# Performance work log

Hardware: AMD Instinct MI355X
Metric: run time of the kernel (lower is better)

## Reference

```python
import jax, jax.numpy as jnp
import numpy as np

INPUT_SIZE = 128
HIDDEN_SIZE = 128
B, S = 4, 4096


def setup_inputs() -> dict:
    key = jax.random.key(0)
    ks = jax.random.split(key, 9)
    sc_in = 1.0 / np.sqrt(INPUT_SIZE)
    sc_h = 1.0 / np.sqrt(HIDDEN_SIZE)
    return {
        "x": jax.random.normal(ks[0], (B, S, INPUT_SIZE), jnp.float32),
        "Wq": jax.random.uniform(ks[1], (INPUT_SIZE, HIDDEN_SIZE), jnp.float32, -sc_in, sc_in),
        "bq": jax.random.uniform(ks[2], (HIDDEN_SIZE,), jnp.float32, -sc_in, sc_in),
        "Wk": jax.random.uniform(ks[3], (INPUT_SIZE, HIDDEN_SIZE), jnp.float32, -sc_in, sc_in),
        "bk": jax.random.uniform(ks[4], (HIDDEN_SIZE,), jnp.float32, -sc_in, sc_in),
        "Wv": jax.random.uniform(ks[5], (INPUT_SIZE, HIDDEN_SIZE), jnp.float32, -sc_in, sc_in),
        "bv": jax.random.uniform(ks[6], (HIDDEN_SIZE,), jnp.float32, -sc_in, sc_in),
        "Wo": jax.random.uniform(ks[7], (HIDDEN_SIZE, INPUT_SIZE), jnp.float32, -sc_h, sc_h),
        "bo": jax.random.uniform(ks[8], (INPUT_SIZE,), jnp.float32, -sc_h, sc_h),
    }


def reference(x, Wq, bq, Wk, bk, Wv, bv, Wo, bo):
    # single-head scaled dot-product attention (non-causal), dropout is eval-mode identity
    q = x @ Wq + bq                      # [B, S, H]
    k = x @ Wk + bk                      # [B, S, H]
    v = x @ Wv + bv                      # [B, S, H]
    scale = 1.0 / jnp.sqrt(jnp.asarray(HIDDEN_SIZE, x.dtype))
    scores = jnp.einsum("bsh,bth->bst", q, k) * scale   # [B, S, S]
    attn = jax.nn.softmax(scores, axis=-1)
    attended = jnp.einsum("bst,bth->bsh", attn, v)       # [B, S, H]
    return attended @ Wo + bo                            # [B, S, input_size]
```

## Files before the change

kernel.cpp:

```cpp
#include <hip/hip_runtime.h>
#include <stdint.h>

typedef __attribute__((ext_vector_type(8))) short short8;
typedef __attribute__((ext_vector_type(4))) float f32x4;
typedef __attribute__((ext_vector_type(16))) float f32x16;
typedef __attribute__((ext_vector_type(4))) int i32x4;
typedef __attribute__((ext_vector_type(2))) int i32x2;

#define MFMA16(a, b, c) __builtin_amdgcn_mfma_f32_16x16x32_bf16((a), (b), (c), 0, 0, 0)
#define MFMA32(a, b, c) __builtin_amdgcn_mfma_f32_32x32x16_bf16((a), (b), (c), 0, 0, 0)

typedef __attribute__((address_space(1))) const void GVoid;
typedef __attribute__((address_space(3))) void LVoid;
#define GLDS16(g, l) __builtin_amdgcn_global_load_lds((GVoid*)(g), (LVoid*)(l), 16, 0, 0)

#define L2E 1.4426950408889634f

__device__ __forceinline__ unsigned short f2bf(float f) {
  unsigned int u = __builtin_bit_cast(unsigned int, f);
  u += 0x7fffu + ((u >> 16) & 1u);
  return (unsigned short)(u >> 16);
}
__device__ __forceinline__ float bf2f(unsigned short u) {
  return __builtin_bit_cast(float, (unsigned int)u << 16);
}

__device__ __forceinline__ float fexp2(float x) {
  return __builtin_amdgcn_exp2f(x);
}

__device__ __forceinline__ i32x2 pls(int a, int b) {
  return __builtin_amdgcn_permlane32_swap(a, b, false, false);
}
__device__ __forceinline__ float fasf(int x) { return __builtin_bit_cast(float, x); }
__device__ __forceinline__ int iasi(float x) { return __builtin_bit_cast(int, x); }

__device__ __forceinline__ int cvtpk(float lo, float hi) {
  int d;
  asm("v_cvt_pk_bf16_f32 %0, %1, %2" : "=v"(d) : "v"(lo), "v"(hi));
  return d;
}

__global__ __launch_bounds__(256) void k_proj(
    const float* __restrict__ x,
    const float* __restrict__ Wq, const float* __restrict__ bq,
    const float* __restrict__ Wk, const float* __restrict__ bk,
    const float* __restrict__ Wv, const float* __restrict__ bv,
    const float* __restrict__ Wo,
    unsigned short* __restrict__ Q2, unsigned short* __restrict__ K2,
    unsigned short* __restrict__ V2, unsigned short* __restrict__ Wo2)
{
  __shared__ __align__(16) unsigned short wt[128 * 128];
  __shared__ __align__(16) unsigned short st[64 * 136];
  const int tid  = threadIdx.x;
  const int lane = tid & 63;
  const int wid  = tid >> 6;
  const int l15  = lane & 15;
  const int g    = lane >> 4;
  const int wI   = blockIdx.x >> 8;
  const int blk  = blockIdx.x & 255;
  const int r0   = blk * 64 + wid * 16;

  if (blockIdx.x == 0) {
    for (int e = tid; e < 16384; e += 256) {
      int j = e & 7, ln = (e >> 3) & 63, kt = (e >> 9) & 7, dt = e >> 12;
      int h = kt * 16 + (ln >> 5) * 8 + j, oc = dt * 32 + (ln & 31);
      Wo2[e] = f2bf(Wo[h * 128 + oc]);
    }
  }

  short8 af[4];
  {
    const float* xp = x + (r0 + l15) * 128 + g * 8;
#pragma unroll
    for (int kt = 0; kt < 4; ++kt) {
      float4 v0 = *(const float4*)(xp + kt * 32);
      float4 v1 = *(const float4*)(xp + kt * 32 + 4);
      short8 a;
      a[0] = (short)f2bf(v0.x); a[1] = (short)f2bf(v0.y);
      a[2] = (short)f2bf(v0.z); a[3] = (short)f2bf(v0.w);
      a[4] = (short)f2bf(v1.x); a[5] = (short)f2bf(v1.y);
      a[6] = (short)f2bf(v1.z); a[7] = (short)f2bf(v1.w);
      af[kt] = a;
    }
  }

  const float* W  = (wI == 0) ? Wq : (wI == 1) ? Wk : Wv;
  const float* bv_ = (wI == 0) ? bq : (wI == 1) ? bk : bv;

  for (int i = 0; i < 64; ++i) {
    int idx = i * 256 + tid;
    int k = idx >> 7, n = idx & 127;
    int cs = (k >> 3) ^ (n & 7);
    wt[n * 128 + cs * 8 + (k & 7)] = f2bf(W[idx]);
  }
  __syncthreads();

  float bias[8];
#pragma unroll
  for (int nt = 0; nt < 8; ++nt) bias[nt] = bv_[nt * 16 + l15];

  f32x4 acc[8];
#pragma unroll
  for (int nt = 0; nt < 8; ++nt) acc[nt] = (f32x4){0.f, 0.f, 0.f, 0.f};

#pragma unroll
  for (int nt = 0; nt < 8; ++nt) {
    const int n = nt * 16 + l15;
#pragma unroll
    for (int ks = 0; ks < 4; ++ks) {
      int cs = (ks * 4 + g) ^ (n & 7);
      short8 bf = *(const short8*)&wt[n * 128 + cs * 8];
      acc[nt] = MFMA16(af[ks], bf, acc[nt]);
    }
  }

  if (wI < 2) {
    const float sc = (wI == 0) ? 0.08838834764831845f : 1.0f;
#pragma unroll
    for (int nt = 0; nt < 8; ++nt) {
      int col = nt * 16 + l15;
#pragma unroll
      for (int r = 0; r < 4; ++r)
        st[(wid * 16 + g * 4 + r) * 136 + col] = f2bf((acc[nt][r] + bias[nt]) * sc);
    }
    __syncthreads();
    unsigned short* Og = (wI == 0) ? Q2 : K2;
#pragma unroll
    for (int c4 = 0; c4 < 4; ++c4) {
      int c = c4 * 256 + tid;
      int T = c >> 9, cc = c & 511;
      int kt = cc >> 6, hib = (cc >> 5) & 1, s32 = cc & 31;
      int m0 = blk * 64 + T * 32;
      int bb = m0 >> 12, tile = (m0 & 4095) >> 5;
      short8 v = *(const short8*)&st[(T * 32 + s32) * 136 + kt * 16 + hib * 8];
      *(short8*)&Og[(size_t)(bb * 128 + tile) * 4096 + cc * 8] = v;
    }
  } else {
#pragma unroll
    for (int nt = 0; nt < 8; ++nt) {
      int col = nt * 16 + l15;
      int m0 = r0 + g * 4;
      int bb = m0 >> 12, srow = m0 & 4095;
      int idx = (bb * 128 + (srow >> 5)) * 4096 + ((srow >> 4) & 1) * 2048 +
                (col >> 5) * 512 + ((srow >> 3) & 1) * 256 + (col & 31) * 8 +
                (srow & 7);
      ushort4 pk;
      pk.x = f2bf(acc[nt][0] + bias[nt]);
      pk.y = f2bf(acc[nt][1] + bias[nt]);
      pk.z = f2bf(acc[nt][2] + bias[nt]);
      pk.w = f2bf(acc[nt][3] + bias[nt]);
      *(ushort4*)&V2[idx] = pk;
    }
  }
}

__global__ __launch_bounds__(256, 2) void k_attn(
    const unsigned short* __restrict__ Q2,
    const unsigned short* __restrict__ K2,
    const unsigned short* __restrict__ V2,
    unsigned short* __restrict__ PA,
    float2* __restrict__ ML2)
{
  __shared__ __align__(16) char smem[66560];
  const int tid = threadIdx.x, lane = tid & 63, wid = tid >> 6;
  const int rr = lane & 31, hi = lane >> 5;
  const int p = blockIdx.x;
  const int b = (p & 7) >> 1;
  const int idx = ((p >> 3) << 1) | (p & 1);
  const int qst = idx >> 2, kvq = idx & 3;
  const int q0tile = qst * 4 + wid;

  short8 qf[8];
  {
    const unsigned short* qp = Q2 + (size_t)(b * 128 + q0tile) * 4096 + lane * 8;
#pragma unroll
    for (int kt = 0; kt < 8; ++kt) qf[kt] = *(const short8*)(qp + kt * 512);
  }

  const unsigned short* gsrc[4];
  gsrc[0] = K2 + (size_t)(b * 128 + kvq * 32 + 0) * 4096 + tid * 8;
  gsrc[1] = K2 + (size_t)(b * 128 + kvq * 32 + 1) * 4096 + tid * 8;
  gsrc[2] = V2 + (size_t)(b * 128 + kvq * 32 + 0) * 4096 + tid * 8;
  gsrc[3] = V2 + (size_t)(b * 128 + kvq * 32 + 1) * 4096 + tid * 8;

  char* const rbuf = smem + 65536 + wid * 128;

#pragma unroll
  for (int i = 0; i < 4; ++i) {
    GLDS16(gsrc[i], smem + i * 8192 + tid * 16);
    GLDS16(gsrc[i] + 2048, smem + i * 8192 + 4096 + tid * 16);
  }

  f32x16 O[4];
#pragma unroll
  for (int dt = 0; dt < 4; ++dt)
#pragma unroll
    for (int j = 0; j < 16; ++j) O[dt][j] = 0.f;
  f32x16 zc;
#pragma unroll
  for (int j = 0; j < 16; ++j) zc[j] = 0.f;
  float mS = -3.0e38f, lS = 0.f;

  for (int t = 0; t < 16; ++t) {
    char* const b0 = smem + (t & 1) * 32768;
    if (t < 15) {
      char* const bn = smem + ((t + 1) & 1) * 32768;
      const size_t adv = (size_t)(t + 1) * 8192;
#pragma unroll
      for (int i = 0; i < 4; ++i) {
        GLDS16(gsrc[i] + adv, bn + i * 8192 + tid * 16);
        GLDS16(gsrc[i] + adv + 2048, bn + i * 8192 + 4096 + tid * 16);
      }
      asm volatile("s_waitcnt vmcnt(8)" ::: "memory");
    } else {
      asm volatile("s_waitcnt vmcnt(0)" ::: "memory");
    }
    __builtin_amdgcn_s_barrier();
    __builtin_amdgcn_sched_barrier(0);

    f32x16 sT0, sT1;
    __builtin_amdgcn_s_setprio(1);
    {
      short8 kf[8];
#pragma unroll
      for (int kt = 0; kt < 8; ++kt)
        kf[kt] = *(const short8*)(b0 + kt * 1024 + lane * 16);
      sT0 = MFMA32(kf[0], qf[0], zc);
#pragma unroll
      for (int kt = 1; kt < 8; ++kt) sT0 = MFMA32(kf[kt], qf[kt], sT0);
    }
    {
      short8 kf[8];
#pragma unroll
      for (int kt = 0; kt < 8; ++kt)
        kf[kt] = *(const short8*)(b0 + 8192 + kt * 1024 + lane * 16);
      sT1 = MFMA32(kf[0], qf[0], zc);
#pragma unroll
      for (int kt = 1; kt < 8; ++kt) sT1 = MFMA32(kf[kt], qf[kt], sT1);
    }
    __builtin_amdgcn_s_setprio(0);

    {
      float pm = fmaxf(fmaxf(fmaxf(sT0[0], sT0[1]), fmaxf(sT0[2], sT0[3])),
                       fmaxf(fmaxf(sT0[4], sT0[5]), fmaxf(sT0[6], sT0[7])));
      pm = fmaxf(pm, fmaxf(fmaxf(fmaxf(sT0[8], sT0[9]), fmaxf(sT0[10], sT0[11])),
                           fmaxf(fmaxf(sT0[12], sT0[13]), fmaxf(sT0[14], sT0[15]))));
      { i32x2 r = pls(iasi(pm), iasi(pm)); pm = fmaxf(fasf(r[0]), fasf(r[1])); }

      if (!__all(pm - mS <= 8.0f)) {
        float mnew = fmaxf(mS, pm);
        float fsc = fexp2((mS - mnew) * L2E);
        mS = mnew;
        lS *= fsc;
        if (hi == 0) *(float*)(rbuf + rr * 4) = fsc;
        f32x4 fr[4];
#pragma unroll
        for (int i = 0; i < 4; ++i)
          fr[i] = *(const f32x4*)(rbuf + i * 32 + hi * 16);
#pragma unroll
        for (int dt = 0; dt < 4; ++dt)
#pragma unroll
          for (int i = 0; i < 4; ++i)
#pragma unroll
            for (int j = 0; j < 4; ++j) O[dt][i * 4 + j] *= fr[i][j];
      }

      const float mL = mS * L2E;
      float pv[16];
#pragma unroll
      for (int r = 0; r < 16; ++r) pv[r] = fexp2(sT0[r] * L2E - mL);
      float s01 = (pv[0] + pv[1]) + (pv[2] + pv[3]);
      float s23 = (pv[4] + pv[5]) + (pv[6] + pv[7]);
      float s45 = (pv[8] + pv[9]) + (pv[10] + pv[11]);
      float s67 = (pv[12] + pv[13]) + (pv[14] + pv[15]);
      float ts = (s01 + s23) + (s45 + s67);
      { i32x2 r = pls(iasi(ts), iasi(ts)); ts = fasf(r[0]) + fasf(r[1]); }
      lS += ts;

      short8 pa0, pa1;
      {
        int dw[8];
#pragma unroll
        for (int m = 0; m < 8; ++m) dw[m] = cvtpk(pv[2 * m], pv[2 * m + 1]);
        i32x2 ra = pls(dw[0], dw[2]);
        i32x2 rb = pls(dw[1], dw[3]);
        i32x2 rc = pls(dw[4], dw[6]);
        i32x2 rd = pls(dw[5], dw[7]);
        i32x4 w0 = {ra[0], rb[0], ra[1], rb[1]};
        i32x4 w1 = {rc[0], rd[0], rc[1], rd[1]};
        pa0 = __builtin_bit_cast(short8, w0);
        pa1 = __builtin_bit_cast(short8, w1);
      }

      __builtin_amdgcn_s_setprio(1);
      {
        const char* vb = b0 + 16384;
        short8 vf[4];
#pragma unroll
        for (int dt = 0; dt < 4; ++dt)
          vf[dt] = *(const short8*)(vb + dt * 1024 + lane * 16);
#pragma unroll
        for (int dt = 0; dt < 4; ++dt) O[dt] = MFMA32(pa0, vf[dt], O[dt]);
#pragma unroll
        for (int dt = 0; dt < 4; ++dt)
          vf[dt] = *(const short8*)(vb + 4096 + dt * 1024 + lane * 16);
#pragma unroll
        for (int dt = 0; dt < 4; ++dt) O[dt] = MFMA32(pa1, vf[dt], O[dt]);
      }
      __builtin_amdgcn_s_setprio(0);
    }

    {
      float pm = fmaxf(fmaxf(fmaxf(sT1[0], sT1[1]), fmaxf(sT1[2], sT1[3])),
                       fmaxf(fmaxf(sT1[4], sT1[5]), fmaxf(sT1[6], sT1[7])));
      pm = fmaxf(pm, fmaxf(fmaxf(fmaxf(sT1[8], sT1[9]), fmaxf(sT1[10], sT1[11])),
                           fmaxf(fmaxf(sT1[12], sT1[13]), fmaxf(sT1[14], sT1[15]))));
      { i32x2 r = pls(iasi(pm), iasi(pm)); pm = fmaxf(fasf(r[0]), fasf(r[1])); }

      if (!__all(pm - mS <= 8.0f)) {
        float mnew = fmaxf(mS, pm);
        float fsc = fexp2((mS - mnew) * L2E);
        mS = mnew;
        lS *= fsc;
        if (hi == 0) *(float*)(rbuf + rr * 4) = fsc;
        f32x4 fr[4];
#pragma unroll
        for (int i = 0; i < 4; ++i)
          fr[i] = *(const f32x4*)(rbuf + i * 32 + hi * 16);
#pragma unroll
        for (int dt = 0; dt < 4; ++dt)
#pragma unroll
          for (int i = 0; i < 4; ++i)
#pragma unroll
            for (int j = 0; j < 4; ++j) O[dt][i * 4 + j] *= fr[i][j];
      }

      const float mL = mS * L2E;
      float pv[16];
#pragma unroll
      for (int r = 0; r < 16; ++r) pv[r] = fexp2(sT1[r] * L2E - mL);
      float s01 = (pv[0] + pv[1]) + (pv[2] + pv[3]);
      float s23 = (pv[4] + pv[5]) + (pv[6] + pv[7]);
      float s45 = (pv[8] + pv[9]) + (pv[10] + pv[11]);
      float s67 = (pv[12] + pv[13]) + (pv[14] + pv[15]);
      float ts = (s01 + s23) + (s45 + s67);
      { i32x2 r = pls(iasi(ts), iasi(ts)); ts = fasf(r[0]) + fasf(r[1]); }
      lS += ts;

      short8 pa2, pa3;
      {
        int dw[8];
#pragma unroll
        for (int m = 0; m < 8; ++m) dw[m] = cvtpk(pv[2 * m], pv[2 * m + 1]);
        i32x2 ra = pls(dw[0], dw[2]);
        i32x2 rb = pls(dw[1], dw[3]);
        i32x2 rc = pls(dw[4], dw[6]);
        i32x2 rd = pls(dw[5], dw[7]);
        i32x4 w0 = {ra[0], rb[0], ra[1], rb[1]};
        i32x4 w1 = {rc[0], rd[0], rc[1], rd[1]};
        pa2 = __builtin_bit_cast(short8, w0);
        pa3 = __builtin_bit_cast(short8, w1);
      }

      __builtin_amdgcn_s_setprio(1);
      {
        const char* vb = b0 + 16384 + 8192;
        short8 vf[4];
#pragma unroll
        for (int dt = 0; dt < 4; ++dt)
          vf[dt] = *(const short8*)(vb + dt * 1024 + lane * 16);
#pragma unroll
        for (int dt = 0; dt < 4; ++dt) O[dt] = MFMA32(pa2, vf[dt], O[dt]);
#pragma unroll
        for (int dt = 0; dt < 4; ++dt)
          vf[dt] = *(const short8*)(vb + 4096 + dt * 1024 + lane * 16);
#pragma unroll
        for (int dt = 0; dt < 4; ++dt) O[dt] = MFMA32(pa3, vf[dt], O[dt]);
      }
      __builtin_amdgcn_s_setprio(0);
    }

    __builtin_amdgcn_s_barrier();
  }

  unsigned short* pab = PA + ((size_t)(b * 4 + kvq) * 128 + q0tile) * 4096;
#pragma unroll
  for (int dt = 0; dt < 4; ++dt) {
    int kt = dt * 2 + (rr >> 4);
#pragma unroll
    for (int r = 0; r < 16; ++r) {
      int q = (r & 3) + 8 * (r >> 2) + 4 * hi;
      int e = kt * 512 + (((rr >> 3) & 1) * 32 + q) * 8 + (rr & 7);
      pab[e] = f2bf(O[dt][r]);
    }
  }
  if (hi == 0)
    ML2[(size_t)(b * 4 + kvq) * 4096 + q0tile * 32 + rr] = make_float2(mS, lS);
}

__global__ __launch_bounds__(256) void k_merge(
    const unsigned short* __restrict__ PA,
    const float2* __restrict__ ML2,
    const unsigned short* __restrict__ Wo2,
    const float* __restrict__ bo,
    float* __restrict__ out)
{
  const int tid = threadIdx.x, lane = tid & 63, w = tid >> 6;
  const int rr = lane & 31, hi = lane >> 5;
  const int p = blockIdx.x;
  const int b = (p & 7) >> 1;
  const int qt32 = ((p >> 3) << 1) | (p & 1);

  float mh[4], lh[4];
#pragma unroll
  for (int h = 0; h < 4; ++h) {
    float2 ml = ML2[(size_t)(b * 4 + h) * 4096 + qt32 * 32 + rr];
    mh[h] = ml.x; lh[h] = ml.y;
  }
  float M = fmaxf(fmaxf(mh[0], mh[1]), fmaxf(mh[2], mh[3]));
  float ch[4], L = 0.f;
#pragma unroll
  for (int h = 0; h < 4; ++h) { ch[h] = fexp2((mh[h] - M) * L2E); L += ch[h] * lh[h]; }
  float iL = 1.0f / L;
#pragma unroll
  for (int h = 0; h < 4; ++h) ch[h] *= iL;

  short8 attb[8];
#pragma unroll
  for (int kt = 0; kt < 8; ++kt) {
    float a[8];
#pragma unroll
    for (int j = 0; j < 8; ++j) a[j] = 0.f;
#pragma unroll
    for (int h = 0; h < 4; ++h) {
      short8 ph = *(const short8*)(PA + ((size_t)(b * 4 + h) * 128 + qt32) * 4096 +
                                   kt * 512 + lane * 8);
#pragma unroll
      for (int j = 0; j < 8; ++j)
        a[j] += ch[h] * bf2f((unsigned short)ph[j]);
    }
    i32x4 wv = {cvtpk(a[0], a[1]), cvtpk(a[2], a[3]),
                cvtpk(a[4], a[5]), cvtpk(a[6], a[7])};
    attb[kt] = __builtin_bit_cast(short8, wv);
  }

  short8 wof[8];
#pragma unroll
  for (int kt = 0; kt < 8; ++kt)
    wof[kt] = *(const short8*)(Wo2 + (w * 8 + kt) * 512 + lane * 8);

  f32x16 zc;
#pragma unroll
  for (int j = 0; j < 16; ++j) zc[j] = 0.f;
  f32x16 acc = MFMA32(attb[0], wof[0], zc);
#pragma unroll
  for (int kt = 1; kt < 8; ++kt) acc = MFMA32(attb[kt], wof[kt], acc);

  float bov = bo[w * 32 + rr];
  float* op = out + (size_t)(b * 4096 + qt32 * 32) * 128 + w * 32 + rr;
#pragma unroll
  for (int r = 0; r < 16; ++r) {
    int q = (r & 3) + 8 * (r >> 2) + 4 * hi;
    op[q * 128] = acc[r] + bov;
  }
}

extern "C" void kernel_launch(void* const* d_in, const int* in_sizes, int n_in,
                              void* d_out, int out_size, void* d_ws, size_t ws_size,
                              hipStream_t stream) {
  const float* x  = (const float*)d_in[0];
  const float* Wq = (const float*)d_in[1];
  const float* bq = (const float*)d_in[2];
  const float* Wk = (const float*)d_in[3];
  const float* bk = (const float*)d_in[4];
  const float* Wv = (const float*)d_in[5];
  const float* bv = (const float*)d_in[6];
  const float* Wo = (const float*)d_in[7];
  const float* bo = (const float*)d_in[8];

  const size_t NE = 4u * 4096u * 128u;
  unsigned short* Q2  = (unsigned short*)d_ws;
  unsigned short* K2  = Q2 + NE;
  unsigned short* V2  = K2 + NE;
  unsigned short* Wo2 = V2 + NE;
  unsigned short* PA  = Wo2 + 16384;
  float2*         ML2 = (float2*)(PA + (size_t)16 * 128 * 4096);

  k_proj<<<768, 256, 0, stream>>>(x, Wq, bq, Wk, bk, Wv, bv, Wo, Q2, K2, V2, Wo2);
  k_attn<<<512, 256, 0, stream>>>(Q2, K2, V2, PA, ML2);
  k_merge<<<512, 256, 0, stream>>>(PA, ML2, Wo2, bo, (float*)d_out);
}
```

Baseline: 76.11 us.

## Fuse split-KV merge and output projection into attention kernel via completion counter

Removes the separate merge kernel. Each attention block now publishes its partial output and softmax statistics, then increments a per-query-tile atomic counter. The last of the four KV-split blocks for a tile combines the partials and applies the Wo projection plus bias, with each wave computing all four output column tiles. This saves a kernel launch and the gap between kernels, but adds a memset launch to clear the counters, memory fences, and serialized tail work on whichever block finishes last.

```diff
diff --git a/kernel.cpp b/kernel.cpp
--- a/kernel.cpp
+++ b/kernel.cpp
@@ -160,7 +160,11 @@
     const unsigned short* __restrict__ K2,
     const unsigned short* __restrict__ V2,
     unsigned short* __restrict__ PA,
-    float2* __restrict__ ML2)
+    float2* __restrict__ ML2,
+    unsigned int* __restrict__ cnt,
+    const unsigned short* __restrict__ Wo2,
+    const float* __restrict__ bo,
+    float* __restrict__ out)
 {
   __shared__ __align__(16) char smem[66560];
   const int tid = threadIdx.x, lane = tid & 63, wid = tid >> 6;
@@ -397,72 +401,70 @@
   }
   if (hi == 0)
     ML2[(size_t)(b * 4 + kvq) * 4096 + q0tile * 32 + rr] = make_float2(mS, lS);
-}
-
-__global__ __launch_bounds__(256) void k_merge(
-    const unsigned short* __restrict__ PA,
-    const float2* __restrict__ ML2,
-    const unsigned short* __restrict__ Wo2,
-    const float* __restrict__ bo,
-    float* __restrict__ out)
-{
-  const int tid = threadIdx.x, lane = tid & 63, w = tid >> 6;
-  const int rr = lane & 31, hi = lane >> 5;
-  const int p = blockIdx.x;
-  const int b = (p & 7) >> 1;
-  const int qt32 = ((p >> 3) << 1) | (p & 1);
-
-  float mh[4], lh[4];
-#pragma unroll
-  for (int h = 0; h < 4; ++h) {
-    float2 ml = ML2[(size_t)(b * 4 + h) * 4096 + qt32 * 32 + rr];
-    mh[h] = ml.x; lh[h] = ml.y;
-  }
-  float M = fmaxf(fmaxf(mh[0], mh[1]), fmaxf(mh[2], mh[3]));
-  float ch[4], L = 0.f;
-#pragma unroll
-  for (int h = 0; h < 4; ++h) { ch[h] = fexp2((mh[h] - M) * L2E); L += ch[h] * lh[h]; }
-  float iL = 1.0f / L;
-#pragma unroll
-  for (int h = 0; h < 4; ++h) ch[h] *= iL;
-
-  short8 attb[8];
-#pragma unroll
-  for (int kt = 0; kt < 8; ++kt) {
-    float a[8];
-#pragma unroll
-    for (int j = 0; j < 8; ++j) a[j] = 0.f;
+
+  __threadfence();
+  __syncthreads();
+  volatile int* flag = (volatile int*)(smem + 66304);
+  if (tid == 0) {
+    unsigned int old = atomicAdd(&cnt[b * 32 + qst], 1u);
+    *flag = (old == 3u) ? 1 : 0;
+  }
+  __syncthreads();
+  if (*flag == 0) return;
+  __threadfence();
+
+  {
+    float mh[4], lh[4];
 #pragma unroll
     for (int h = 0; h < 4; ++h) {
-      short8 ph = *(const short8*)(PA + ((size_t)(b * 4 + h) * 128 + qt32) * 4096 +
-                                   kt * 512 + lane * 8);
-#pragma unroll
-      for (int j = 0; j < 8; ++j)
-        a[j] += ch[h] * bf2f((unsigned short)ph[j]);
-    }
-    i32x4 wv = {cvtpk(a[0], a[1]), cvtpk(a[2], a[3]),
-                cvtpk(a[4], a[5]), cvtpk(a[6], a[7])};
-    attb[kt] = __builtin_bit_cast(short8, wv);
-  }
-
-  short8 wof[8];
-#pragma unroll
-  for (int kt = 0; kt < 8; ++kt)
-    wof[kt] = *(const short8*)(Wo2 + (w * 8 + kt) * 512 + lane * 8);
-
-  f32x16 zc;
-#pragma unroll
-  for (int j = 0; j < 16; ++j) zc[j] = 0.f;
-  f32x16 acc = MFMA32(attb[0], wof[0], zc);
-#pragma unroll
-  for (int kt = 1; kt < 8; ++kt) acc = MFMA32(attb[kt], wof[kt], acc);
-
-  float bov = bo[w * 32 + rr];
-  float* op = out + (size_t)(b * 4096 + qt32 * 32) * 128 + w * 32 + rr;
-#pragma unroll
-  for (int r = 0; r < 16; ++r) {
-    int q = (r & 3) + 8 * (r >> 2) + 4 * hi;
-    op[q * 128] = acc[r] + bov;
+      float2 ml = ML2[(size_t)(b * 4 + h) * 4096 + q0tile * 32 + rr];
+      mh[h] = ml.x; lh[h] = ml.y;
+    }
+    float M = fmaxf(fmaxf(mh[0], mh[1]), fmaxf(mh[2], mh[3]));
+    float ch[4], L = 0.f;
+#pragma unroll
+    for (int h = 0; h < 4; ++h) { ch[h] = fexp2((mh[h] - M) * L2E); L += ch[h] * lh[h]; }
+    float iL = 1.0f / L;
+#pragma unroll
+    for (int h = 0; h < 4; ++h) ch[h] *= iL;
+
+    short8 attb[8];
+#pragma unroll
+    for (int kt = 0; kt < 8; ++kt) {
+      float a[8];
+#pragma unroll
+      for (int j = 0; j < 8; ++j) a[j] = 0.f;
+#pragma unroll
+      for (int h = 0; h < 4; ++h) {
+        short8 ph = *(const short8*)(PA + ((size_t)(b * 4 + h) * 128 + q0tile) * 4096 +
+                                     kt * 512 + lane * 8);
+#pragma unroll
+        for (int j = 0; j < 8; ++j)
+          a[j] += ch[h] * bf2f((unsigned short)ph[j]);
+      }
+      i32x4 wv = {cvtpk(a[0], a[1]), cvtpk(a[2], a[3]),
+                  cvtpk(a[4], a[5]), cvtpk(a[6], a[7])};
+      attb[kt] = __builtin_bit_cast(short8, wv);
+    }
+
+#pragma unroll
+    for (int w4 = 0; w4 < 4; ++w4) {
+      short8 wof[8];
+#pragma unroll
+      for (int kt = 0; kt < 8; ++kt)
+        wof[kt] = *(const short8*)(Wo2 + (w4 * 8 + kt) * 512 + lane * 8);
+      f32x16 acc = MFMA32(attb[0], wof[0], zc);
+#pragma unroll
+      for (int kt = 1; kt < 8; ++kt) acc = MFMA32(attb[kt], wof[kt], acc);
+
+      float bov = bo[w4 * 32 + rr];
+      float* op = out + (size_t)(b * 4096 + q0tile * 32) * 128 + w4 * 32 + rr;
+#pragma unroll
+      for (int r = 0; r < 16; ++r) {
+        int q = (r & 3) + 8 * (r >> 2) + 4 * hi;
+        op[q * 128] = acc[r] + bov;
+      }
+    }
   }
 }
 
@@ -486,8 +488,9 @@
   unsigned short* Wo2 = V2 + NE;
   unsigned short* PA  = Wo2 + 16384;
   float2*         ML2 = (float2*)(PA + (size_t)16 * 128 * 4096);
-
+  unsigned int*   cnt = (unsigned int*)(ML2 + (size_t)16 * 4096);
+
+  hipMemsetAsync(cnt, 0, 128 * sizeof(unsigned int), stream);
   k_proj<<<768, 256, 0, stream>>>(x, Wq, bq, Wk, bk, Wv, bv, Wo, Q2, K2, V2, Wo2);
-  k_attn<<<512, 256, 0, stream>>>(Q2, K2, V2, PA, ML2);
-  k_merge<<<512, 256, 0, stream>>>(PA, ML2, Wo2, bo, (float*)d_out);
-}
+  k_attn<<<512, 256, 0, stream>>>(Q2, K2, V2, PA, ML2, cnt, Wo2, bo, (float*)d_out);
+}
```

Result: slower. 186.8 us (+145.5%).
